# Kernel optimization log

Measured on AMD Instinct MI355X. Metric: run time of the kernel, lower is better.

## Reference

```python
import jax, jax.numpy as jnp
import numpy as np

INPUT_DIM = 256
OUTPUT_DIM = 512
NUM_KNOTS = 64
RANGE_KNOTS = (-1.0, 1.0)
DEGREE = 3
BATCH = 4096


def bspline_basis(x, knots, degree):
    """Cox-de Boor recursion. x: [B, I], knots: [K] (uniform, ascending).
    Returns basis values [B, I, K - degree - 1]."""
    xe = x[..., None]  # [B, I, 1]
    # degree-0: indicator of knot interval k, k = 0..K-2
    basis = ((xe >= knots[:-1]) & (xe < knots[1:])).astype(x.dtype)  # [B, I, K-1]
    for d in range(1, degree + 1):
        k = np.arange(knots.shape[0] - d - 1)
        left = (xe - knots[k]) / (knots[k + d] - knots[k]) * basis[..., :-1]
        right = (knots[k + d + 1] - xe) / (knots[k + d + 1] - knots[k + 1]) * basis[..., 1:]
        basis = left + right  # [B, I, K-d-1]
    return basis


def setup_inputs() -> dict:
    key = jax.random.key(0)
    kx, kb, ks = jax.random.split(key, 3)
    x = jax.random.uniform(kx, (BATCH, INPUT_DIM), dtype=jnp.float32)
    wb = jax.random.uniform(kb, (INPUT_DIM, OUTPUT_DIM), dtype=jnp.float32)
    ws = jax.random.uniform(ks, (INPUT_DIM, OUTPUT_DIM), dtype=jnp.float32)
    cps = jnp.ones((INPUT_DIM, NUM_KNOTS), dtype=jnp.float32)
    knots = jnp.asarray(np.linspace(RANGE_KNOTS[0], RANGE_KNOTS[1], NUM_KNOTS), dtype=jnp.float32)
    return {"x": x, "wb": wb, "ws": ws, "cps": cps, "knots": knots}


def reference(x, wb, ws, cps, knots):
    num_basis = NUM_KNOTS - DEGREE - 1
    basis = bspline_basis(x, knots, DEGREE)            # [B, I, num_basis]
    # per-input-dim spline value: sum_k cps[i, k] * B_k(x[b, i])
    spline = jnp.einsum('bik,ik->bi', basis, cps[:, :num_basis])  # [B, I]
    base = jax.nn.silu(x)                               # [B, I]
    # out[b, o] = sum_i wb[i, o] * silu(x[b, i]) + ws[i, o] * spline[b, i]
    out = base @ wb + spline @ ws                       # [B, O]
    return out
```

## Files before the change

### kernel.cpp

```cpp
#include <hip/hip_runtime.h>
#include <hip/hip_bf16.h>

#define BATCH    4096
#define IN_DIM   256
#define OUT_DIM  512
#define KDIM     512
#define NKNOTS   64
#define NBASIS   60

typedef __attribute__((ext_vector_type(8))) short bf16x8;
typedef __attribute__((ext_vector_type(4))) float f32x4;

__device__ __forceinline__ short f2bf(float f) {
    __hip_bfloat16 h = __float2bfloat16(f);
    return *reinterpret_cast<short*>(&h);
}
__device__ __forceinline__ float bf2f(short s) {
    __hip_bfloat16 h = *reinterpret_cast<__hip_bfloat16*>(&s);
    return __bfloat162float(h);
}

__global__ __launch_bounds__(256) void prep_kernel(
        const float* __restrict__ x, const float* __restrict__ wb,
        const float* __restrict__ ws, const float* __restrict__ cps,
        const float* __restrict__ knots,
        short* __restrict__ A, short* __restrict__ Bt) {
    __shared__ short cpsT[NKNOTS * IN_DIM];
    __shared__ float tile[64 * 65];

    const int tid = threadIdx.x;
    const int bid = blockIdx.x;

    if (bid < 256) {
        for (int k4 = 0; k4 < NKNOTS; k4 += 4) {
            float4 v = *(const float4*)&cps[tid * NKNOTS + k4];
            cpsT[(k4 + 0) * IN_DIM + tid] = f2bf(v.x);
            cpsT[(k4 + 1) * IN_DIM + tid] = f2bf(v.y);
            cpsT[(k4 + 2) * IN_DIM + tid] = f2bf(v.z);
            cpsT[(k4 + 3) * IN_DIM + tid] = f2bf(v.w);
        }
        __syncthreads();

        for (int it = 0; it < 16; ++it) {
            int e = (bid * 16 + it) * 256 + tid;
            int b = e >> 8;
            int i = e & (IN_DIM - 1);

            float xv = x[e];
            float base = xv / (1.0f + __expf(-xv));

            float u = (xv + 1.0f) * 31.5f;
            int   j = (int)floorf(u);
            float spline = 0.0f;
            if (j >= 0 && j <= 62) {
                float t  = (xv - knots[j]) * 31.5f;
                float t2 = t * t, t3 = t2 * t;
                float omt = 1.0f - t;
                const float c6 = 1.0f / 6.0f;
                float w0 = omt * omt * omt * c6;
                float w1 = (3.0f*t3 - 6.0f*t2 + 4.0f) * c6;
                float w2 = (-3.0f*t3 + 3.0f*t2 + 3.0f*t + 1.0f) * c6;
                float w3 = t3 * c6;
                int k0 = j - 3;
                if (k0     >= 0 && k0     < NBASIS) spline += w0 * bf2f(cpsT[(k0    ) * IN_DIM + i]);
                if (k0 + 1 >= 0 && k0 + 1 < NBASIS) spline += w1 * bf2f(cpsT[(k0 + 1) * IN_DIM + i]);
                if (k0 + 2 >= 0 && k0 + 2 < NBASIS) spline += w2 * bf2f(cpsT[(k0 + 2) * IN_DIM + i]);
                if (k0 + 3 >= 0 && k0 + 3 < NBASIS) spline += w3 * bf2f(cpsT[(k0 + 3) * IN_DIM + i]);
            }
            A[b * KDIM + i]          = f2bf(base);
            A[b * KDIM + IN_DIM + i] = f2bf(spline);
        }
    } else {
        int t = bid - 256;
        const float* W = (t & 32) ? ws : wb;
        int koffs = (t & 32) ? IN_DIM : 0;
        int kb = ((t >> 3) & 3) * 64;
        int nb = (t & 7) * 64;

        for (int it = 0; it < 16; ++it) {
            int f = it * 256 + tid;
            int r = f >> 6, c = f & 63;
            tile[r * 65 + c] = W[(kb + r) * OUT_DIM + nb + c];
        }
        __syncthreads();
        for (int it = 0; it < 16; ++it) {
            int f = it * 256 + tid;
            int n = f >> 6, k = f & 63;
            Bt[(nb + n) * KDIM + koffs + kb + k] = f2bf(tile[k * 65 + n]);
        }
    }
}

#define BM 64
#define BN 64
#define BK 64

#define GLOAD_LDS16(g, l)                                                  \
    __builtin_amdgcn_global_load_lds(                                      \
        (const __attribute__((address_space(1))) void*)(g),                \
        (__attribute__((address_space(3))) void*)(l), 16, 0, 0)

__global__ __launch_bounds__(256) void gemm_kernel(
        const short* __restrict__ A, const short* __restrict__ Bt,
        float* __restrict__ C) {
    __shared__ __align__(16) short As[BM * BK];
    __shared__ __align__(16) short Bs[BN * BK];

    const int tid  = threadIdx.x;
    const int lane = tid & 63;
    const int wave = tid >> 6;
    const int m0 = blockIdx.y * BM;
    const int n0 = blockIdx.x * BN;
    const int wm = (wave & 1) * 32;
    const int wn = (wave >> 1) * 32;
    const int fr = lane & 15;
    const int q  = lane >> 4;

    const int lrow = lane >> 3;
    const int c_sw = (lane & 7) ^ lrow;
    const int ra0 = wave * 16 + lrow;
    const int ra1 = wave * 16 + 8 + lrow;

    f32x4 acc[2][2] = {};

    for (int k0 = 0; k0 < KDIM; k0 += BK) {
        GLOAD_LDS16(&A [(m0 + ra0) * KDIM + k0 + c_sw * 8], &As[(wave * 2    ) * 512]);
        GLOAD_LDS16(&A [(m0 + ra1) * KDIM + k0 + c_sw * 8], &As[(wave * 2 + 1) * 512]);
        GLOAD_LDS16(&Bt[(n0 + ra0) * KDIM + k0 + c_sw * 8], &Bs[(wave * 2    ) * 512]);
        GLOAD_LDS16(&Bt[(n0 + ra1) * KDIM + k0 + c_sw * 8], &Bs[(wave * 2 + 1) * 512]);
        __syncthreads();

        #pragma unroll
        for (int kk = 0; kk < 2; ++kk) {
            const int ck = kk * 4 + q;
            const int sw = (ck ^ (fr & 7)) * 8;
            bf16x8 a0 = *(const bf16x8*)&As[(wm + fr)      * BK + sw];
            bf16x8 a1 = *(const bf16x8*)&As[(wm + 16 + fr) * BK + sw];
            bf16x8 b0 = *(const bf16x8*)&Bs[(wn + fr)      * BK + sw];
            bf16x8 b1 = *(const bf16x8*)&Bs[(wn + 16 + fr) * BK + sw];
            acc[0][0] = __builtin_amdgcn_mfma_f32_16x16x32_bf16(a0, b0, acc[0][0], 0, 0, 0);
            acc[0][1] = __builtin_amdgcn_mfma_f32_16x16x32_bf16(a0, b1, acc[0][1], 0, 0, 0);
            acc[1][0] = __builtin_amdgcn_mfma_f32_16x16x32_bf16(a1, b0, acc[1][0], 0, 0, 0);
            acc[1][1] = __builtin_amdgcn_mfma_f32_16x16x32_bf16(a1, b1, acc[1][1], 0, 0, 0);
        }
        __syncthreads();
    }

    const int rbase = q * 4;
    #pragma unroll
    for (int mt = 0; mt < 2; ++mt) {
        #pragma unroll
        for (int nt = 0; nt < 2; ++nt) {
            #pragma unroll
            for (int r = 0; r < 4; ++r) {
                int row = m0 + wm + mt * 16 + rbase + r;
                int col = n0 + wn + nt * 16 + fr;
                C[row * OUT_DIM + col] = acc[mt][nt][r];
            }
        }
    }
}

extern "C" void kernel_launch(void* const* d_in, const int* in_sizes, int n_in,
                              void* d_out, int out_size, void* d_ws, size_t ws_size,
                              hipStream_t stream) {
    const float* x     = (const float*)d_in[0];
    const float* wb    = (const float*)d_in[1];
    const float* ws    = (const float*)d_in[2];
    const float* cps   = (const float*)d_in[3];
    const float* knots = (const float*)d_in[4];
    float* out = (float*)d_out;

    short* Abf = (short*)d_ws;
    short* Btb = (short*)((char*)d_ws + (size_t)BATCH * KDIM * 2);

    prep_kernel<<<320, 256, 0, stream>>>(x, wb, ws, cps, knots, Abf, Btb);

    dim3 grid(OUT_DIM / BN, BATCH / BM);
    gemm_kernel<<<grid, 256, 0, stream>>>(Abf, Btb, out);
}
```

Measured before the change: 84.81 us.

## Fuse prep and GEMM into one cooperative kernel with grid sync

Merges the activation/spline prep kernel and the bf16 MFMA GEMM into a single cooperative launch of 512 blocks. Each block first optionally transposes a weight tile, builds its share of the A matrix, then does a grid-wide sync before computing one 64x64 output tile. This removes one kernel launch and the gap between launches. In exchange it adds the cost of a grid barrier, and every block must now convert the full cps table to bf16 in LDS, which is redundant work. The 48KB of shared memory per block may also limit how many blocks fit at once for the cooperative launch.

```diff
diff --git a/kernel.cpp b/kernel.cpp
--- a/kernel.cpp
+++ b/kernel.cpp
@@ -1,5 +1,8 @@
 #include <hip/hip_runtime.h>
 #include <hip/hip_bf16.h>
+#include <hip/hip_cooperative_groups.h>
+
+namespace cg = cooperative_groups;
 
 #define BATCH    4096
 #define IN_DIM   256
@@ -20,62 +23,33 @@
     return __bfloat162float(h);
 }
 
-__global__ __launch_bounds__(256) void prep_kernel(
+#define GLOAD_LDS16(g, l)                                                  \
+    __builtin_amdgcn_global_load_lds(                                      \
+        (const __attribute__((address_space(1))) void*)(g),                \
+        (__attribute__((address_space(3))) void*)(l), 16, 0, 0)
+
+__global__ __launch_bounds__(256) void fused_kernel(
         const float* __restrict__ x, const float* __restrict__ wb,
         const float* __restrict__ ws, const float* __restrict__ cps,
         const float* __restrict__ knots,
-        short* __restrict__ A, short* __restrict__ Bt) {
-    __shared__ short cpsT[NKNOTS * IN_DIM];
-    __shared__ float tile[64 * 65];
+        short* __restrict__ A, short* __restrict__ Bt,
+        float* __restrict__ C) {
+    __shared__ __align__(16) char shmem[49152];
+    short* cpsT = (short*)shmem;
+    float* tile = (float*)shmem;
+    short* As   = (short*)(shmem + 32768);
+    short* Bs   = (short*)(shmem + 40960);
 
     const int tid = threadIdx.x;
     const int bid = blockIdx.x;
+    const int lane = tid & 63;
+    const int wave = tid >> 6;
 
-    if (bid < 256) {
-        for (int k4 = 0; k4 < NKNOTS; k4 += 4) {
-            float4 v = *(const float4*)&cps[tid * NKNOTS + k4];
-            cpsT[(k4 + 0) * IN_DIM + tid] = f2bf(v.x);
-            cpsT[(k4 + 1) * IN_DIM + tid] = f2bf(v.y);
-            cpsT[(k4 + 2) * IN_DIM + tid] = f2bf(v.z);
-            cpsT[(k4 + 3) * IN_DIM + tid] = f2bf(v.w);
-        }
-        __syncthreads();
-
-        for (int it = 0; it < 16; ++it) {
-            int e = (bid * 16 + it) * 256 + tid;
-            int b = e >> 8;
-            int i = e & (IN_DIM - 1);
-
-            float xv = x[e];
-            float base = xv / (1.0f + __expf(-xv));
-
-            float u = (xv + 1.0f) * 31.5f;
-            int   j = (int)floorf(u);
-            float spline = 0.0f;
-            if (j >= 0 && j <= 62) {
-                float t  = (xv - knots[j]) * 31.5f;
-                float t2 = t * t, t3 = t2 * t;
-                float omt = 1.0f - t;
-                const float c6 = 1.0f / 6.0f;
-                float w0 = omt * omt * omt * c6;
-                float w1 = (3.0f*t3 - 6.0f*t2 + 4.0f) * c6;
-                float w2 = (-3.0f*t3 + 3.0f*t2 + 3.0f*t + 1.0f) * c6;
-                float w3 = t3 * c6;
-                int k0 = j - 3;
-                if (k0     >= 0 && k0     < NBASIS) spline += w0 * bf2f(cpsT[(k0    ) * IN_DIM + i]);
-                if (k0 + 1 >= 0 && k0 + 1 < NBASIS) spline += w1 * bf2f(cpsT[(k0 + 1) * IN_DIM + i]);
-                if (k0 + 2 >= 0 && k0 + 2 < NBASIS) spline += w2 * bf2f(cpsT[(k0 + 2) * IN_DIM + i]);
-                if (k0 + 3 >= 0 && k0 + 3 < NBASIS) spline += w3 * bf2f(cpsT[(k0 + 3) * IN_DIM + i]);
-            }
-            A[b * KDIM + i]          = f2bf(base);
-            A[b * KDIM + IN_DIM + i] = f2bf(spline);
-        }
-    } else {
-        int t = bid - 256;
-        const float* W = (t & 32) ? ws : wb;
-        int koffs = (t & 32) ? IN_DIM : 0;
-        int kb = ((t >> 3) & 3) * 64;
-        int nb = (t & 7) * 64;
+    if (bid < 64) {
+        const float* W = (bid & 32) ? ws : wb;
+        int koffs = (bid & 32) ? IN_DIM : 0;
+        int kb = ((bid >> 3) & 3) * 64;
+        int nb = (bid & 7) * 64;
 
         for (int it = 0; it < 16; ++it) {
             int f = it * 256 + tid;
@@ -88,29 +62,52 @@
             int n = f >> 6, k = f & 63;
             Bt[(nb + n) * KDIM + koffs + kb + k] = f2bf(tile[k * 65 + n]);
         }
+        __syncthreads();
     }
-}
 
-#define BM 64
-#define BN 64
-#define BK 64
+    for (int k4 = 0; k4 < NKNOTS; k4 += 4) {
+        float4 v = *(const float4*)&cps[tid * NKNOTS + k4];
+        cpsT[(k4 + 0) * IN_DIM + tid] = f2bf(v.x);
+        cpsT[(k4 + 1) * IN_DIM + tid] = f2bf(v.y);
+        cpsT[(k4 + 2) * IN_DIM + tid] = f2bf(v.z);
+        cpsT[(k4 + 3) * IN_DIM + tid] = f2bf(v.w);
+    }
+    __syncthreads();
 
-#define GLOAD_LDS16(g, l)                                                  \
-    __builtin_amdgcn_global_load_lds(                                      \
-        (const __attribute__((address_space(1))) void*)(g),                \
-        (__attribute__((address_space(3))) void*)(l), 16, 0, 0)
+    for (int it = 0; it < 8; ++it) {
+        int e = bid * 2048 + it * 256 + tid;
+        int b = e >> 8;
+        int i = e & (IN_DIM - 1);
 
-__global__ __launch_bounds__(256) void gemm_kernel(
-        const short* __restrict__ A, const short* __restrict__ Bt,
-        float* __restrict__ C) {
-    __shared__ __align__(16) short As[BM * BK];
-    __shared__ __align__(16) short Bs[BN * BK];
+        float xv = x[e];
+        float base = xv / (1.0f + __expf(-xv));
 
-    const int tid  = threadIdx.x;
-    const int lane = tid & 63;
-    const int wave = tid >> 6;
-    const int m0 = blockIdx.y * BM;
-    const int n0 = blockIdx.x * BN;
+        float u = (xv + 1.0f) * 31.5f;
+        int   j = (int)floorf(u);
+        float spline = 0.0f;
+        if (j >= 0 && j <= 62) {
+            float t  = (xv - knots[j]) * 31.5f;
+            float t2 = t * t, t3 = t2 * t;
+            float omt = 1.0f - t;
+            const float c6 = 1.0f / 6.0f;
+            float w0 = omt * omt * omt * c6;
+            float w1 = (3.0f*t3 - 6.0f*t2 + 4.0f) * c6;
+            float w2 = (-3.0f*t3 + 3.0f*t2 + 3.0f*t + 1.0f) * c6;
+            float w3 = t3 * c6;
+            int k0 = j - 3;
+            if (k0     >= 0 && k0     < NBASIS) spline += w0 * bf2f(cpsT[(k0    ) * IN_DIM + i]);
+            if (k0 + 1 >= 0 && k0 + 1 < NBASIS) spline += w1 * bf2f(cpsT[(k0 + 1) * IN_DIM + i]);
+            if (k0 + 2 >= 0 && k0 + 2 < NBASIS) spline += w2 * bf2f(cpsT[(k0 + 2) * IN_DIM + i]);
+            if (k0 + 3 >= 0 && k0 + 3 < NBASIS) spline += w3 * bf2f(cpsT[(k0 + 3) * IN_DIM + i]);
+        }
+        A[b * KDIM + i]          = f2bf(base);
+        A[b * KDIM + IN_DIM + i] = f2bf(spline);
+    }
+
+    cg::this_grid().sync();
+
+    const int m0 = (bid >> 3) * 64;
+    const int n0 = (bid & 7) * 64;
     const int wm = (wave & 1) * 32;
     const int wn = (wave >> 1) * 32;
     const int fr = lane & 15;
@@ -123,7 +120,7 @@
 
     f32x4 acc[2][2] = {};
 
-    for (int k0 = 0; k0 < KDIM; k0 += BK) {
+    for (int k0 = 0; k0 < KDIM; k0 += 64) {
         GLOAD_LDS16(&A [(m0 + ra0) * KDIM + k0 + c_sw * 8], &As[(wave * 2    ) * 512]);
         GLOAD_LDS16(&A [(m0 + ra1) * KDIM + k0 + c_sw * 8], &As[(wave * 2 + 1) * 512]);
         GLOAD_LDS16(&Bt[(n0 + ra0) * KDIM + k0 + c_sw * 8], &Bs[(wave * 2    ) * 512]);
@@ -134,10 +131,10 @@
         for (int kk = 0; kk < 2; ++kk) {
             const int ck = kk * 4 + q;
             const int sw = (ck ^ (fr & 7)) * 8;
-            bf16x8 a0 = *(const bf16x8*)&As[(wm + fr)      * BK + sw];
-            bf16x8 a1 = *(const bf16x8*)&As[(wm + 16 + fr) * BK + sw];
-            bf16x8 b0 = *(const bf16x8*)&Bs[(wn + fr)      * BK + sw];
-            bf16x8 b1 = *(const bf16x8*)&Bs[(wn + 16 + fr) * BK + sw];
+            bf16x8 a0 = *(const bf16x8*)&As[(wm + fr)      * 64 + sw];
+            bf16x8 a1 = *(const bf16x8*)&As[(wm + 16 + fr) * 64 + sw];
+            bf16x8 b0 = *(const bf16x8*)&Bs[(wn + fr)      * 64 + sw];
+            bf16x8 b1 = *(const bf16x8*)&Bs[(wn + 16 + fr) * 64 + sw];
             acc[0][0] = __builtin_amdgcn_mfma_f32_16x16x32_bf16(a0, b0, acc[0][0], 0, 0, 0);
             acc[0][1] = __builtin_amdgcn_mfma_f32_16x16x32_bf16(a0, b1, acc[0][1], 0, 0, 0);
             acc[1][0] = __builtin_amdgcn_mfma_f32_16x16x32_bf16(a1, b0, acc[1][0], 0, 0, 0);
@@ -174,8 +171,8 @@
     short* Abf = (short*)d_ws;
     short* Btb = (short*)((char*)d_ws + (size_t)BATCH * KDIM * 2);
 
-    prep_kernel<<<320, 256, 0, stream>>>(x, wb, ws, cps, knots, Abf, Btb);
-
-    dim3 grid(OUT_DIM / BN, BATCH / BM);
-    gemm_kernel<<<grid, 256, 0, stream>>>(Abf, Btb, out);
+    void* args[] = {(void*)&x, (void*)&wb, (void*)&ws, (void*)&cps,
+                    (void*)&knots, (void*)&Abf, (void*)&Btb, (void*)&out};
+    hipLaunchCooperativeKernel((const void*)fused_kernel, dim3(512), dim3(256),
+                               args, 0, stream);
 }
```

New measurement: 139.5 us. 1.64x slower.
